# Optimization experiments

Hardware: AMD Instinct MI355X
Metric: run time of the kernel (lower is better)

## Reference

```python
import jax, jax.numpy as jnp
import numpy as np

B, T, D = 2, 2048, 1024
H, HD = 16, 64
DL, DC = 512, 256
THETA = 10000.0
LN_EPS = 1e-5


def setup_inputs() -> dict:
    key = jax.random.key(0)
    ks = jax.random.split(key, 8)
    s = 0.02
    return {
        "x": jax.random.normal(ks[0], (B, T, D), jnp.float32),
        "W_q": jax.random.normal(ks[1], (H * HD, D), jnp.float32) * s,
        "b_q": jnp.zeros((H * HD,), jnp.float32),
        "W_kvl": jax.random.normal(ks[2], (DL, D), jnp.float32) * s,
        "b_kvl": jnp.zeros((DL,), jnp.float32),
        "ts_scale": jnp.ones((DL,), jnp.float32),
        "ts_shift": jnp.zeros((DL,), jnp.float32),
        "W_comp": jax.random.normal(ks[3], (DC, DL), jnp.float32) * s,
        "W_exp": jax.random.normal(ks[4], (DL, DC), jnp.float32) * s,
        "ln_g": jnp.ones((DC,), jnp.float32),
        "ln_b": jnp.zeros((DC,), jnp.float32),
        "W_fkv": jax.random.normal(ks[5], (2 * H * HD, DL), jnp.float32) * s,
        "b_fkv": jnp.zeros((2 * H * HD,), jnp.float32),
        "W_out": jax.random.normal(ks[6], (D, H * HD), jnp.float32) * s,
        "b_out": jnp.zeros((D,), jnp.float32),
    }


def _rope_tables(t_len):
    inv_freq = 1.0 / (THETA ** (jnp.arange(0, HD, 2, dtype=jnp.float32) / HD))
    pos = jnp.arange(t_len, dtype=jnp.float32)
    freqs = pos[:, None] * inv_freq[None, :]          # [T, HD/2]
    cos = jnp.concatenate([jnp.cos(freqs)] * 2, -1)   # [T, HD]
    sin = jnp.concatenate([jnp.sin(freqs)] * 2, -1)
    return cos[None, None], sin[None, None]           # [1,1,T,HD]


def _rotate_half(z):
    return jnp.concatenate([-z[..., HD // 2:], z[..., :HD // 2]], -1)


def reference(x, W_q, b_q, W_kvl, b_kvl, ts_scale, ts_shift, W_comp, W_exp,
              ln_g, ln_b, W_fkv, b_fkv, W_out, b_out):
    # Q path: [B,T,D] -> [B,H,T,HD]
    q = (jnp.einsum('btd,ed->bte', x, W_q) + b_q).reshape(B, T, H, HD).transpose(0, 2, 1, 3)

    # KV latent + learned KVSplice bottleneck
    kvl = jnp.einsum('btd,ld->btl', x, W_kvl) + b_kvl                 # [B,T,DL]
    xt = kvl * jax.nn.softplus(ts_scale) + ts_shift
    c = jnp.einsum('btl,cl->btc', xt, W_comp)                         # [B,T,DC]
    mu = jnp.mean(c, -1, keepdims=True)
    var = jnp.mean(jnp.square(c - mu), -1, keepdims=True)
    c = (c - mu) * jax.lax.rsqrt(var + LN_EPS) * ln_g + ln_b
    dec = jnp.einsum('btc,lc->btl', c, W_exp)                         # [B,T,DL]

    # Decompress latent to K,V
    kv = jnp.einsum('btl,el->bte', dec, W_fkv) + b_fkv                # [B,T,2*H*HD]
    kv = kv.reshape(B, T, 2, H, HD).transpose(2, 0, 3, 1, 4)          # [2,B,H,T,HD]
    k, v = kv[0], kv[1]

    # RoPE
    cos, sin = _rope_tables(T)
    q = q * cos + _rotate_half(q) * sin
    k = k * cos + _rotate_half(k) * sin

    # Causal SDPA
    scale = 1.0 / np.sqrt(HD)
    scores = jnp.einsum('bhqd,bhkd->bhqk', q, k) * scale
    mask = jnp.tril(jnp.ones((T, T), bool))
    scores = jnp.where(mask, scores, jnp.float32(-1e30))
    attn = jax.nn.softmax(scores, axis=-1)
    o = jnp.einsum('bhqk,bhkd->bhqd', attn, v)
    o = o.transpose(0, 2, 1, 3).reshape(B, T, H * HD)
    return jnp.einsum('bte,de->btd', o, W_out) + b_out
```

## Files before the change

### kernel.cpp

```cpp
#include <hip/hip_runtime.h>
#include <math.h>

#define B_SZ   2
#define T_SEQ  2048
#define NH     16
#define HDIM   64
#define D_MOD  1024
#define DL     512
#define DC     256
#define MROWS  4096

typedef __attribute__((ext_vector_type(8))) short bf16x8;
typedef __attribute__((ext_vector_type(4))) float f32x4;

#define SCALE_Q 0.18033688011112042f

static __device__ __forceinline__ unsigned short f2bf(float f) {
    union { float f; unsigned u; } v; v.f = f;
    unsigned r = v.u + 0x7fffu + ((v.u >> 16) & 1u);
    return (unsigned short)(r >> 16);
}

static __device__ __forceinline__ void gl_lds16(const unsigned short* g,
                                                unsigned short* l) {
    __builtin_amdgcn_global_load_lds(
        (const __attribute__((address_space(1))) unsigned int*)g,
        (__attribute__((address_space(3))) unsigned int*)l, 16, 0, 0);
}

__global__ __launch_bounds__(256) void cvt_bf16(
    const float* __restrict__ x,  const float* __restrict__ wq,
    const float* __restrict__ wkvl, const float* __restrict__ wcomp,
    const float* __restrict__ wexp, const float* __restrict__ wfkv,
    const float* __restrict__ wout,
    unsigned short* __restrict__ xb,  unsigned short* __restrict__ wqh,
    unsigned short* __restrict__ wkvlh, unsigned short* __restrict__ wcomph,
    unsigned short* __restrict__ wexph, unsigned short* __restrict__ wfkvh,
    unsigned short* __restrict__ wouth, float2* __restrict__ rope_tab)
{
    const int g = blockIdx.x * 256 + threadIdx.x;
    const int stride = gridDim.x * 256;
#define CVT_SEG(src, dst, n4)                                              \
    for (int i = g; i < (n4); i += stride) {                               \
        float4 v = ((const float4*)(src))[i];                              \
        unsigned short h[4] = {f2bf(v.x), f2bf(v.y), f2bf(v.z), f2bf(v.w)};\
        *(uint2*)((dst) + (size_t)i * 4) = *(uint2*)h;                     \
    }
    CVT_SEG(x, xb, 1048576)
    CVT_SEG(wq, wqh, 262144)
    CVT_SEG(wkvl, wkvlh, 131072)
    CVT_SEG(wcomp, wcomph, 32768)
    CVT_SEG(wexp, wexph, 32768)
    CVT_SEG(wfkv, wfkvh, 262144)
    CVT_SEG(wout, wouth, 262144)
#undef CVT_SEG
    for (int i = g; i < T_SEQ * 32; i += stride) {
        const int t = i >> 5, fi = i & 31;
        const float inv = __expf((float)fi * (-9.210340371976184f / 32.0f));
        float sn, cs; sincosf((float)t * inv, &sn, &cs);
        rope_tab[i] = make_float2(cs, sn);
    }
}

#define GEMM64R_PROLOG(Aptr, Wptr, Kdim)                                       \
    __shared__ unsigned short As[64 * 64];                                     \
    __shared__ unsigned short Ws[64 * 64];                                     \
    const int tid = threadIdx.x;                                               \
    const int w = tid >> 6, lane = tid & 63;                                   \
    const int l16 = lane & 15, quad = lane >> 4;                               \
    const int sw8 = ((lane & 7) ^ ((lane >> 3) & 7)) << 3;                     \
    const int srow = lane >> 3;                                                \
    const unsigned short* Ag0 = (Aptr) + (size_t)(m0 + w * 16 + srow) * (Kdim) + sw8;      \
    const unsigned short* Ag1 = (Aptr) + (size_t)(m0 + w * 16 + 8 + srow) * (Kdim) + sw8;  \
    const unsigned short* Wg0 = (Wptr) + (size_t)(n0 + w * 16 + srow) * (Kdim) + sw8;      \
    const unsigned short* Wg1 = (Wptr) + (size_t)(n0 + w * 16 + 8 + srow) * (Kdim) + sw8;  \
    unsigned short* Al0 = &As[(w * 16) * 64];                                  \
    unsigned short* Al1 = &As[(w * 16 + 8) * 64];                              \
    unsigned short* Wl0 = &Ws[(w * 16) * 64];                                  \
    unsigned short* Wl1 = &Ws[(w * 16 + 8) * 64];                              \
    const int xh = (l16 & 7);                                                  \
    f32x4 acc[4];                                                              \
    _Pragma("unroll") for (int j = 0; j < 4; ++j)                              \
        acc[j] = (f32x4){0.f, 0.f, 0.f, 0.f};                                  \
    for (int k0 = 0; k0 < (Kdim); k0 += 64) {                                  \
        __syncthreads();                                                       \
        gl_lds16(Ag0 + k0, Al0);                                               \
        gl_lds16(Ag1 + k0, Al1);                                               \
        gl_lds16(Wg0 + k0, Wl0);                                               \
        gl_lds16(Wg1 + k0, Wl1);                                               \
        __syncthreads();                                                       \
        bf16x8 af[2], bfr[4][2];                                               \
        _Pragma("unroll") for (int kk = 0; kk < 2; ++kk)                       \
            af[kk] = *(const bf16x8*)&As[(w * 16 + l16) * 64 +                 \
                                         (((kk * 4 + quad) ^ xh) << 3)];       \
        _Pragma("unroll") for (int j = 0; j < 4; ++j)                          \
            _Pragma("unroll") for (int kk = 0; kk < 2; ++kk)                   \
                bfr[j][kk] = *(const bf16x8*)&Ws[(j * 16 + l16) * 64 +         \
                                             (((kk * 4 + quad) ^ xh) << 3)];   \
        _Pragma("unroll") for (int kk = 0; kk < 2; ++kk)                       \
            _Pragma("unroll") for (int j = 0; j < 4; ++j)                      \
                acc[j] = __builtin_amdgcn_mfma_f32_16x16x32_bf16(              \
                    af[kk], bfr[j][kk], acc[j], 0, 0, 0);                      \
    }

__global__ __launch_bounds__(256) void gemm_qxt(
    const unsigned short* __restrict__ A, const unsigned short* __restrict__ Wq,
    const unsigned short* __restrict__ Wkvl,
    const float* __restrict__ b_q, const float* __restrict__ b_kvl,
    const float* __restrict__ ts_scale, const float* __restrict__ ts_shift,
    const float2* __restrict__ tab,
    unsigned short* __restrict__ qh, unsigned short* __restrict__ xt)
{
    const int m0 = blockIdx.x * 64;
    const bool is_q = (blockIdx.y < 16);
    const int n0 = is_q ? blockIdx.y * 64 : (blockIdx.y - 16) * 64;
    const unsigned short* W = is_q ? Wq : Wkvl;

    GEMM64R_PROLOG(A, W, D_MOD)

    if (is_q) {
#pragma unroll
        for (int j = 0; j < 4; ++j) {
            const int col = n0 + j * 16 + l16;
            const int h = col >> 6, hd = col & 63;
            const float bv = b_q[col];
            const float bvp = b_q[col ^ 32];
            const float sgn = (hd < 32) ? -1.f : 1.f;
#pragma unroll
            for (int reg = 0; reg < 4; ++reg) {
                const int row = m0 + w * 16 + quad * 4 + reg;
                const int b = row >> 11, t = row & (T_SEQ - 1);
                const float2 cssn = tab[t * 32 + (hd & 31)];
                const float v  = acc[j][reg] + bv;
                const float vp = acc[j ^ 2][reg] + bvp;
                const float r = (v * cssn.x + sgn * vp * cssn.y) * SCALE_Q;
                qh[(((size_t)b * NH + h) * T_SEQ + t) * HDIM + hd] = f2bf(r);
            }
        }
    } else {
#pragma unroll
        for (int j = 0; j < 4; ++j) {
            const int col = n0 + j * 16 + l16;
            const float bv = b_kvl[col];
            const float sp_s = log1pf(expf(ts_scale[col]));
            const float sp_t = ts_shift[col];
#pragma unroll
            for (int reg = 0; reg < 4; ++reg) {
                const int row = m0 + w * 16 + quad * 4 + reg;
                const float val = (acc[j][reg] + bv) * sp_s + sp_t;
                xt[(size_t)row * DL + col] = f2bf(val);
            }
        }
    }
}

__global__ __launch_bounds__(256) void gemm_kv(
    const unsigned short* __restrict__ A, const unsigned short* __restrict__ W,
    const float* __restrict__ bias, const float2* __restrict__ tab,
    unsigned short* __restrict__ kh, unsigned short* __restrict__ vth)
{
    const int m0 = blockIdx.x * 64, n0 = blockIdx.y * 64;

    GEMM64R_PROLOG(A, W, DL)

    if (n0 < 1024) {
#pragma unroll
        for (int j = 0; j < 4; ++j) {
            const int col = n0 + j * 16 + l16;
            const int h = (col >> 6) & 15, hd = col & 63;
            const float bv = bias[col];
            const float bvp = bias[col ^ 32];
            const float sgn = (hd < 32) ? -1.f : 1.f;
#pragma unroll
            for (int reg = 0; reg < 4; ++reg) {
                const int row = m0 + w * 16 + quad * 4 + reg;
                const int b = row >> 11, t = row & (T_SEQ - 1);
                const float2 cssn = tab[t * 32 + (hd & 31)];
                const float v  = acc[j][reg] + bv;
                const float vp = acc[j ^ 2][reg] + bvp;
                const float r = v * cssn.x + sgn * vp * cssn.y;
                kh[(((size_t)b * NH + h) * T_SEQ + t) * HDIM + hd] = f2bf(r);
            }
        }
    } else {
#pragma unroll
        for (int j = 0; j < 4; ++j) {
            const int col = n0 + j * 16 + l16;
            const int cv = col - 1024;
            const int h = cv >> 6, hd = cv & 63;
            const float bv = bias[col];
            unsigned short hv[4];
            const int r0 = m0 + w * 16 + quad * 4;
            const int b = r0 >> 11, t0 = r0 & (T_SEQ - 1);
#pragma unroll
            for (int reg = 0; reg < 4; ++reg)
                hv[reg] = f2bf(acc[j][reg] + bv);
            *(uint2*)&vth[(((size_t)b * NH + h) * HDIM + hd) * T_SEQ + t0] =
                *(uint2*)hv;
        }
    }
}

__global__ __launch_bounds__(256) void gemm_out(
    const unsigned short* __restrict__ A, const unsigned short* __restrict__ W,
    const float* __restrict__ bias, float* __restrict__ C)
{
    const int m0 = blockIdx.x * 64, n0 = blockIdx.y * 64;

    GEMM64R_PROLOG(A, W, D_MOD)

#pragma unroll
    for (int j = 0; j < 4; ++j) {
        const int col = n0 + j * 16 + l16;
        const float bv = bias[col];
#pragma unroll
        for (int reg = 0; reg < 4; ++reg) {
            const int row = m0 + w * 16 + quad * 4 + reg;
            C[(size_t)row * D_MOD + col] = acc[j][reg] + bv;
        }
    }
}

__global__ __launch_bounds__(256) void gemm_b(
    const unsigned short* __restrict__ A, const unsigned short* __restrict__ W,
    unsigned short* __restrict__ dec)
{
    const int m0 = blockIdx.x * 64, n0 = blockIdx.y * 64;

    GEMM64R_PROLOG(A, W, DC)

#pragma unroll
    for (int j = 0; j < 4; ++j) {
        const int col = n0 + j * 16 + l16;
#pragma unroll
        for (int reg = 0; reg < 4; ++reg) {
            const int row = m0 + w * 16 + quad * 4 + reg;
            dec[(size_t)row * DL + col] = f2bf(acc[j][reg]);
        }
    }
}

__global__ __launch_bounds__(256) void gemm_c_ln(
    const unsigned short* __restrict__ A, const unsigned short* __restrict__ W,
    const float* __restrict__ g, const float* __restrict__ bta,
    unsigned short* __restrict__ outb)
{
    __shared__ unsigned short As[16 * 32];
    __shared__ unsigned short Ws[256 * 32];
    __shared__ float redS[4][16];
    __shared__ float redQ[4][16];

    const int tid = threadIdx.x;
    const int w = tid >> 6, lane = tid & 63;
    const int l16 = lane & 15, quad = lane >> 4;
    const int m0 = blockIdx.x * 16;

    const int srow = lane >> 2, scol = (lane & 3) << 3;
    const unsigned short* Ag = A + (size_t)(m0 + srow) * DL + scol;
    const unsigned short* Wg = W + (size_t)(w * 64 + srow) * DL + scol;

    f32x4 acc[4];
#pragma unroll
    for (int j = 0; j < 4; ++j) acc[j] = (f32x4){0.f, 0.f, 0.f, 0.f};

    for (int k0 = 0; k0 < DL; k0 += 32) {
        __syncthreads();
        if (w == 0) gl_lds16(Ag + k0, &As[0]);
#pragma unroll
        for (int c = 0; c < 4; ++c)
            gl_lds16(Wg + (size_t)(c * 16) * DL + k0, &Ws[(w * 64 + c * 16) * 32]);
        __syncthreads();

        const bf16x8 af = *(const bf16x8*)&As[l16 * 32 + quad * 8];
        bf16x8 bfr[4];
#pragma unroll
        for (int j = 0; j < 4; ++j)
            bfr[j] = *(const bf16x8*)&Ws[(w * 64 + j * 16 + l16) * 32 + quad * 8];
#pragma unroll
        for (int j = 0; j < 4; ++j)
            acc[j] = __builtin_amdgcn_mfma_f32_16x16x32_bf16(af, bfr[j], acc[j], 0, 0, 0);
    }

    float s[4], q2[4];
#pragma unroll
    for (int reg = 0; reg < 4; ++reg) {
        float sv = (acc[0][reg] + acc[1][reg]) + (acc[2][reg] + acc[3][reg]);
        float qv = (acc[0][reg] * acc[0][reg] + acc[1][reg] * acc[1][reg]) +
                   (acc[2][reg] * acc[2][reg] + acc[3][reg] * acc[3][reg]);
#pragma unroll
        for (int off = 1; off < 16; off <<= 1) {
            sv += __shfl_xor(sv, off);
            qv += __shfl_xor(qv, off);
        }
        s[reg] = sv; q2[reg] = qv;
    }
    if (l16 == 0) {
#pragma unroll
        for (int reg = 0; reg < 4; ++reg) {
            redS[w][quad * 4 + reg] = s[reg];
            redQ[w][quad * 4 + reg] = q2[reg];
        }
    }
    __syncthreads();

#pragma unroll
    for (int reg = 0; reg < 4; ++reg) {
        const int r = quad * 4 + reg;
        const float sum = (redS[0][r] + redS[1][r]) + (redS[2][r] + redS[3][r]);
        const float sq  = (redQ[0][r] + redQ[1][r]) + (redQ[2][r] + redQ[3][r]);
        const float mu  = sum * (1.0f / DC);
        const float var = sq * (1.0f / DC) - mu * mu;
        const float rstd = rsqrtf(var + 1e-5f);
#pragma unroll
        for (int j = 0; j < 4; ++j) {
            const int col = w * 64 + j * 16 + l16;
            const float val = (acc[j][reg] - mu) * rstd * g[col] + bta[col];
            outb[(size_t)(m0 + r) * DC + col] = f2bf(val);
        }
    }
}

__global__ __launch_bounds__(256, 3) void flash_mfma(
    const unsigned short* __restrict__ q, const unsigned short* __restrict__ k,
    const unsigned short* __restrict__ vt, unsigned short* __restrict__ o)
{
    __shared__ unsigned short Ks[64 * 72];
    __shared__ unsigned short Vs[64 * 72];
    __shared__ unsigned short Ps[64 * 72];

    const int bh = blockIdx.x & 31;
    const int j  = 31 - (blockIdx.x >> 5);
    const int q0 = j * 64;
    const int tid = threadIdx.x;
    const int w = tid >> 6, lane = tid & 63;
    const int l16 = lane & 15, quad = lane >> 4;
    const int rbase = q0 + w * 16;

    bf16x8 qf[2];
#pragma unroll
    for (int kk = 0; kk < 2; ++kk)
        qf[kk] = *(const bf16x8*)(q + ((size_t)bh * T_SEQ + rbase + l16) * HDIM + kk * 32 + quad * 8);

    f32x4 of[4];
    float lrow[4];
#pragma unroll
    for (int dt = 0; dt < 4; ++dt) of[dt] = (f32x4){0.f, 0.f, 0.f, 0.f};
#pragma unroll
    for (int r = 0; r < 4; ++r) lrow[r] = 0.f;

    const int ldr = tid >> 2;
    const int ldc = (tid & 3) * 16;
    const unsigned short* kgb = k + ((size_t)bh * T_SEQ + ldr) * HDIM + ldc;
    const unsigned short* vgb = vt + ((size_t)bh * HDIM + ldr) * T_SEQ + ldc;

    const int kend = (j + 1) * 64;
    for (int k0 = 0; k0 < kend; k0 += 64) {
        __syncthreads();
        {
            const unsigned short* kg = kgb + (size_t)k0 * HDIM;
            *(bf16x8*)&Ks[ldr * 72 + ldc]     = *(const bf16x8*)kg;
            *(bf16x8*)&Ks[ldr * 72 + ldc + 8] = *(const bf16x8*)(kg + 8);
            const unsigned short* vg = vgb + k0;
            *(bf16x8*)&Vs[ldr * 72 + ldc]     = *(const bf16x8*)vg;
            *(bf16x8*)&Vs[ldr * 72 + ldc + 8] = *(const bf16x8*)(vg + 8);
        }
        __syncthreads();

        bf16x8 kf[4][2];
#pragma unroll
        for (int nt = 0; nt < 4; ++nt)
#pragma unroll
            for (int kk = 0; kk < 2; ++kk)
                kf[nt][kk] = *(const bf16x8*)&Ks[(nt * 16 + l16) * 72 + kk * 32 + quad * 8];

        f32x4 sf[4];
#pragma unroll
        for (int nt = 0; nt < 4; ++nt) {
            sf[nt] = (f32x4){0.f, 0.f, 0.f, 0.f};
#pragma unroll
            for (int kk = 0; kk < 2; ++kk)
                sf[nt] = __builtin_amdgcn_mfma_f32_16x16x32_bf16(qf[kk], kf[nt][kk], sf[nt], 0, 0, 0);
        }

        const bool need_mask = (k0 + 63) > rbase;
#pragma unroll
        for (int reg = 0; reg < 4; ++reg) {
            float a0 = sf[0][reg], a1 = sf[1][reg], a2 = sf[2][reg], a3 = sf[3][reg];
            if (need_mask) {
                const int tq = rbase + quad * 4 + reg;
                if (k0 +      l16 > tq) a0 = -1e30f;
                if (k0 + 16 + l16 > tq) a1 = -1e30f;
                if (k0 + 32 + l16 > tq) a2 = -1e30f;
                if (k0 + 48 + l16 > tq) a3 = -1e30f;
            }
            union { float f; unsigned u; } u0, u1, u2, u3;
            u0.f = exp2f(a0); u1.f = exp2f(a1);
            u2.f = exp2f(a2); u3.f = exp2f(a3);
            const int prow = (w * 16 + quad * 4 + reg) * 72 + l16;
            Ps[prow]      = (unsigned short)(u0.u >> 16);
            Ps[prow + 16] = (unsigned short)(u1.u >> 16);
            Ps[prow + 32] = (unsigned short)(u2.u >> 16);
            Ps[prow + 48] = (unsigned short)(u3.u >> 16);
            u0.u &= 0xffff0000u; u1.u &= 0xffff0000u;
            u2.u &= 0xffff0000u; u3.u &= 0xffff0000u;
            lrow[reg] += (u0.f + u1.f) + (u2.f + u3.f);
        }

        bf16x8 vf[4][2];
#pragma unroll
        for (int dt = 0; dt < 4; ++dt)
#pragma unroll
            for (int kk = 0; kk < 2; ++kk)
                vf[dt][kk] = *(const bf16x8*)&Vs[(dt * 16 + l16) * 72 + kk * 32 + quad * 8];

        bf16x8 pf[2];
#pragma unroll
        for (int kk = 0; kk < 2; ++kk)
            pf[kk] = *(const bf16x8*)&Ps[(w * 16 + l16) * 72 + kk * 32 + quad * 8];
#pragma unroll
        for (int dt = 0; dt < 4; ++dt)
#pragma unroll
            for (int kk = 0; kk < 2; ++kk)
                of[dt] = __builtin_amdgcn_mfma_f32_16x16x32_bf16(pf[kk], vf[dt][kk], of[dt], 0, 0, 0);
    }

    const int b = bh >> 4, h = bh & 15;
#pragma unroll
    for (int reg = 0; reg < 4; ++reg) {
        float l = lrow[reg];
        l += __shfl_xor(l, 1);
        l += __shfl_xor(l, 2);
        l += __shfl_xor(l, 4);
        l += __shfl_xor(l, 8);
        const float inv = 1.0f / l;
        const int t = rbase + quad * 4 + reg;
#pragma unroll
        for (int dt = 0; dt < 4; ++dt)
            o[((size_t)b * T_SEQ + t) * (NH * HDIM) + h * HDIM + dt * 16 + l16] =
                f2bf(of[dt][reg] * inv);
    }
}

extern "C" void kernel_launch(void* const* d_in, const int* in_sizes, int n_in,
                              void* d_out, int out_size, void* d_ws, size_t ws_size,
                              hipStream_t stream)
{
    (void)in_sizes; (void)n_in; (void)out_size; (void)ws_size;

    const float* x        = (const float*)d_in[0];
    const float* W_q      = (const float*)d_in[1];
    const float* b_q      = (const float*)d_in[2];
    const float* W_kvl    = (const float*)d_in[3];
    const float* b_kvl    = (const float*)d_in[4];
    const float* ts_scale = (const float*)d_in[5];
    const float* ts_shift = (const float*)d_in[6];
    const float* W_comp   = (const float*)d_in[7];
    const float* W_exp    = (const float*)d_in[8];
    const float* ln_g     = (const float*)d_in[9];
    const float* ln_b     = (const float*)d_in[10];
    const float* W_fkv    = (const float*)d_in[11];
    const float* b_fkv    = (const float*)d_in[12];
    const float* W_out    = (const float*)d_in[13];
    const float* b_out    = (const float*)d_in[14];
    float* out = (float*)d_out;

    char* p = (char*)d_ws;
    unsigned short* xb     = (unsigned short*)p;             p += 8  * 1024 * 1024;
    unsigned short* wqh    = (unsigned short*)p;             p += 2  * 1024 * 1024;
    unsigned short* wkvlh  = (unsigned short*)p;             p += 1  * 1024 * 1024;
    unsigned short* wcomph = (unsigned short*)p;             p += 256 * 1024;
    unsigned short* wexph  = (unsigned short*)p;             p += 256 * 1024;
    unsigned short* wfkvh  = (unsigned short*)p;             p += 2  * 1024 * 1024;
    unsigned short* wouth  = (unsigned short*)p;             p += 2  * 1024 * 1024;
    unsigned short* qh     = (unsigned short*)p;             p += 8  * 1024 * 1024;
    unsigned short* kh     = (unsigned short*)p;             p += 8  * 1024 * 1024;
    unsigned short* vth    = (unsigned short*)p;             p += 8  * 1024 * 1024;
    unsigned short* xt     = (unsigned short*)p;             p += 4  * 1024 * 1024;
    unsigned short* cbh    = (unsigned short*)p;             p += 2  * 1024 * 1024;
    unsigned short* dec    = (unsigned short*)p;             p += 4  * 1024 * 1024;
    unsigned short* ob     = (unsigned short*)p;             p += 8  * 1024 * 1024;
    float2*         tab    = (float2*)p;                     p += 512 * 1024;

    const dim3 blk(256);

    cvt_bf16<<<1024, blk, 0, stream>>>(x, W_q, W_kvl, W_comp, W_exp, W_fkv, W_out,
                                       xb, wqh, wkvlh, wcomph, wexph, wfkvh, wouth,
                                       tab);

    gemm_qxt<<<dim3(64, 24), blk, 0, stream>>>(
        xb, wqh, wkvlh, b_q, b_kvl, ts_scale, ts_shift, tab, qh, xt);

    gemm_c_ln<<<256, blk, 0, stream>>>(
        xt, wcomph, ln_g, ln_b, cbh);

    gemm_b<<<dim3(64, 8), blk, 0, stream>>>(
        cbh, wexph, dec);

    gemm_kv<<<dim3(64, 32), blk, 0, stream>>>(
        dec, wfkvh, b_fkv, tab, kh, vth);

    flash_mfma<<<1024, blk, 0, stream>>>(qh, kh, vth, ob);

    gemm_out<<<dim3(64, 16), blk, 0, stream>>>(
        ob, wouth, b_out, out);
}
```

Measured before the change: 220.9 us.

## Move Q projection into KV GEMM launch, widen LN GEMM k-step, rebalance flash order

The Q projection leaves the first GEMM and is merged into the K/V decompression GEMM launch. The serial chain xt→c→dec now carries fewer blocks, and the K/V launch gets more blocks to fill the GPU. The compress+LayerNorm GEMM now loads 64-wide k-tiles with an XOR-swizzled LDS layout, which halves its loop iterations and reduces bank conflicts. The flash attention block order is changed to interleave heavy and light causal query tiles so the load is better balanced across waves.

Result: no change. 222.8 us (+0.8%).

```diff
diff --git a/kernel.cpp b/kernel.cpp
--- a/kernel.cpp
+++ b/kernel.cpp
@@ -62,9 +62,11 @@
     }
 }
 
+#define GEMM64R_SHARED                                                         \
+    __shared__ unsigned short As[64 * 64];                                     \
+    __shared__ unsigned short Ws[64 * 64];
+
 #define GEMM64R_PROLOG(Aptr, Wptr, Kdim)                                       \
-    __shared__ unsigned short As[64 * 64];                                     \
-    __shared__ unsigned short Ws[64 * 64];                                     \
     const int tid = threadIdx.x;                                               \
     const int w = tid >> 6, lane = tid & 63;                                   \
     const int l16 = lane & 15, quad = lane >> 4;                               \
@@ -103,101 +105,105 @@
                     af[kk], bfr[j][kk], acc[j], 0, 0, 0);                      \
     }
 
-__global__ __launch_bounds__(256) void gemm_qxt(
-    const unsigned short* __restrict__ A, const unsigned short* __restrict__ Wq,
-    const unsigned short* __restrict__ Wkvl,
-    const float* __restrict__ b_q, const float* __restrict__ b_kvl,
+#define Q_EPILOGUE                                                             \
+    _Pragma("unroll") for (int j = 0; j < 4; ++j) {                            \
+        const int col = n0 + j * 16 + l16;                                     \
+        const int h = col >> 6, hd = col & 63;                                 \
+        const float bv = b_q[col];                                             \
+        const float bvp = b_q[col ^ 32];                                       \
+        const float sgn = (hd < 32) ? -1.f : 1.f;                              \
+        _Pragma("unroll") for (int reg = 0; reg < 4; ++reg) {                  \
+            const int row = m0 + w * 16 + quad * 4 + reg;                      \
+            const int b = row >> 11, t = row & (T_SEQ - 1);                    \
+            const float2 cssn = tab[t * 32 + (hd & 31)];                       \
+            const float v  = acc[j][reg] + bv;                                 \
+            const float vp = acc[j ^ 2][reg] + bvp;                            \
+            const float r = (v * cssn.x + sgn * vp * cssn.y) * SCALE_Q;        \
+            qh[(((size_t)b * NH + h) * T_SEQ + t) * HDIM + hd] = f2bf(r);      \
+        }                                                                      \
+    }
+
+__global__ __launch_bounds__(256) void gemm_xt(
+    const unsigned short* __restrict__ A, const unsigned short* __restrict__ W,
+    const float* __restrict__ b_kvl,
     const float* __restrict__ ts_scale, const float* __restrict__ ts_shift,
-    const float2* __restrict__ tab,
-    unsigned short* __restrict__ qh, unsigned short* __restrict__ xt)
-{
+    unsigned short* __restrict__ xt)
+{
+    GEMM64R_SHARED
+    const int m0 = blockIdx.x * 64, n0 = blockIdx.y * 64;
+
+    GEMM64R_PROLOG(A, W, D_MOD)
+
+#pragma unroll
+    for (int j = 0; j < 4; ++j) {
+        const int col = n0 + j * 16 + l16;
+        const float bv = b_kvl[col];
+        const float sp_s = log1pf(expf(ts_scale[col]));
+        const float sp_t = ts_shift[col];
+#pragma unroll
+        for (int reg = 0; reg < 4; ++reg) {
+            const int row = m0 + w * 16 + quad * 4 + reg;
+            const float val = (acc[j][reg] + bv) * sp_s + sp_t;
+            xt[(size_t)row * DL + col] = f2bf(val);
+        }
+    }
+}
+
+__global__ __launch_bounds__(256) void gemm_kvq(
+    const unsigned short* __restrict__ dec, const unsigned short* __restrict__ Wfkv,
+    const float* __restrict__ b_fkv,
+    const unsigned short* __restrict__ xb, const unsigned short* __restrict__ Wq,
+    const float* __restrict__ b_q, const float2* __restrict__ tab,
+    unsigned short* __restrict__ kh, unsigned short* __restrict__ vth,
+    unsigned short* __restrict__ qh)
+{
+    GEMM64R_SHARED
     const int m0 = blockIdx.x * 64;
-    const bool is_q = (blockIdx.y < 16);
-    const int n0 = is_q ? blockIdx.y * 64 : (blockIdx.y - 16) * 64;
-    const unsigned short* W = is_q ? Wq : Wkvl;
-
-    GEMM64R_PROLOG(A, W, D_MOD)
-
-    if (is_q) {
-#pragma unroll
-        for (int j = 0; j < 4; ++j) {
-            const int col = n0 + j * 16 + l16;
-            const int h = col >> 6, hd = col & 63;
-            const float bv = b_q[col];
-            const float bvp = b_q[col ^ 32];
-            const float sgn = (hd < 32) ? -1.f : 1.f;
-#pragma unroll
-            for (int reg = 0; reg < 4; ++reg) {
-                const int row = m0 + w * 16 + quad * 4 + reg;
-                const int b = row >> 11, t = row & (T_SEQ - 1);
-                const float2 cssn = tab[t * 32 + (hd & 31)];
-                const float v  = acc[j][reg] + bv;
-                const float vp = acc[j ^ 2][reg] + bvp;
-                const float r = (v * cssn.x + sgn * vp * cssn.y) * SCALE_Q;
-                qh[(((size_t)b * NH + h) * T_SEQ + t) * HDIM + hd] = f2bf(r);
+    const int y = blockIdx.y;
+
+    if (y < 32) {
+        const int n0 = y * 64;
+        GEMM64R_PROLOG(dec, Wfkv, DL)
+        if (n0 < 1024) {
+#pragma unroll
+            for (int j = 0; j < 4; ++j) {
+                const int col = n0 + j * 16 + l16;
+                const int h = (col >> 6) & 15, hd = col & 63;
+                const float bv = b_fkv[col];
+                const float bvp = b_fkv[col ^ 32];
+                const float sgn = (hd < 32) ? -1.f : 1.f;
+#pragma unroll
+                for (int reg = 0; reg < 4; ++reg) {
+                    const int row = m0 + w * 16 + quad * 4 + reg;
+                    const int b = row >> 11, t = row & (T_SEQ - 1);
+                    const float2 cssn = tab[t * 32 + (hd & 31)];
+                    const float v  = acc[j][reg] + bv;
+                    const float vp = acc[j ^ 2][reg] + bvp;
+                    const float r = v * cssn.x + sgn * vp * cssn.y;
+                    kh[(((size_t)b * NH + h) * T_SEQ + t) * HDIM + hd] = f2bf(r);
+                }
             }
+        } else {
+#pragma unroll
+            for (int j = 0; j < 4; ++j) {
+                const int col = n0 + j * 16 + l16;
+                const int cv = col - 1024;
+                const int h = cv >> 6, hd = cv & 63;
+                const float bv = b_fkv[col];
+                unsigned short hv[4];
+                const int r0 = m0 + w * 16 + quad * 4;
+                const int b = r0 >> 11, t0 = r0 & (T_SEQ - 1);
+#pragma unroll
+                for (int reg = 0; reg < 4; ++reg)
+                    hv[reg] = f2bf(acc[j][reg] + bv);
+                *(uint2*)&vth[(((size_t)b * NH + h) * HDIM + hd) * T_SEQ + t0] =
+                    *(uint2*)hv;
+            }
         }
     } else {
-#pragma unroll
-        for (int j = 0; j < 4; ++j) {
-            const int col = n0 + j * 16 + l16;
-            const float bv = b_kvl[col];
-            const float sp_s = log1pf(expf(ts_scale[col]));
-            const float sp_t = ts_shift[col];
-#pragma unroll
-            for (int reg = 0; reg < 4; ++reg) {
-                const int row = m0 + w * 16 + quad * 4 + reg;
-                const float val = (acc[j][reg] + bv) * sp_s + sp_t;
-                xt[(size_t)row * DL + col] = f2bf(val);
-            }
-        }
-    }
-}
-
-__global__ __launch_bounds__(256) void gemm_kv(
-    const unsigned short* __restrict__ A, const unsigned short* __restrict__ W,
-    const float* __restrict__ bias, const float2* __restrict__ tab,
-    unsigned short* __restrict__ kh, unsigned short* __restrict__ vth)
-{
-    const int m0 = blockIdx.x * 64, n0 = blockIdx.y * 64;
-
-    GEMM64R_PROLOG(A, W, DL)
-
-    if (n0 < 1024) {
-#pragma unroll
-        for (int j = 0; j < 4; ++j) {
-            const int col = n0 + j * 16 + l16;
-            const int h = (col >> 6) & 15, hd = col & 63;
-            const float bv = bias[col];
-            const float bvp = bias[col ^ 32];
-            const float sgn = (hd < 32) ? -1.f : 1.f;
-#pragma unroll
-            for (int reg = 0; reg < 4; ++reg) {
-                const int row = m0 + w * 16 + quad * 4 + reg;
-                const int b = row >> 11, t = row & (T_SEQ - 1);
-                const float2 cssn = tab[t * 32 + (hd & 31)];
-                const float v  = acc[j][reg] + bv;
-                const float vp = acc[j ^ 2][reg] + bvp;
-                const float r = v * cssn.x + sgn * vp * cssn.y;
-                kh[(((size_t)b * NH + h) * T_SEQ + t) * HDIM + hd] = f2bf(r);
-            }
-        }
-    } else {
-#pragma unroll
-        for (int j = 0; j < 4; ++j) {
-            const int col = n0 + j * 16 + l16;
-            const int cv = col - 1024;
-            const int h = cv >> 6, hd = cv & 63;
-            const float bv = bias[col];
-            unsigned short hv[4];
-            const int r0 = m0 + w * 16 + quad * 4;
-            const int b = r0 >> 11, t0 = r0 & (T_SEQ - 1);
-#pragma unroll
-            for (int reg = 0; reg < 4; ++reg)
-                hv[reg] = f2bf(acc[j][reg] + bv);
-            *(uint2*)&vth[(((size_t)b * NH + h) * HDIM + hd) * T_SEQ + t0] =
-                *(uint2*)hv;
-        }
+        const int n0 = (y - 32) * 64;
+        GEMM64R_PROLOG(xb, Wq, D_MOD)
+        Q_EPILOGUE
     }
 }
 
@@ -205,6 +211,7 @@
     const unsigned short* __restrict__ A, const unsigned short* __restrict__ W,
     const float* __restrict__ bias, float* __restrict__ C)
 {
+    GEMM64R_SHARED
     const int m0 = blockIdx.x * 64, n0 = blockIdx.y * 64;
 
     GEMM64R_PROLOG(A, W, D_MOD)
@@ -225,6 +232,7 @@
     const unsigned short* __restrict__ A, const unsigned short* __restrict__ W,
     unsigned short* __restrict__ dec)
 {
+    GEMM64R_SHARED
     const int m0 = blockIdx.x * 64, n0 = blockIdx.y * 64;
 
     GEMM64R_PROLOG(A, W, DC)
@@ -245,8 +253,8 @@
     const float* __restrict__ g, const float* __restrict__ bta,
     unsigned short* __restrict__ outb)
 {
-    __shared__ unsigned short As[16 * 32];
-    __shared__ unsigned short Ws[256 * 32];
+    __shared__ unsigned short As[16 * 64];
+    __shared__ unsigned short Ws[256 * 64];
     __shared__ float redS[4][16];
     __shared__ float redQ[4][16];
 
@@ -255,30 +263,45 @@
     const int l16 = lane & 15, quad = lane >> 4;
     const int m0 = blockIdx.x * 16;
 
-    const int srow = lane >> 2, scol = (lane & 3) << 3;
-    const unsigned short* Ag = A + (size_t)(m0 + srow) * DL + scol;
-    const unsigned short* Wg = W + (size_t)(w * 64 + srow) * DL + scol;
+    const int sw8 = ((lane & 7) ^ ((lane >> 3) & 7)) << 3;
+    const int srow = lane >> 3;
+    const int xh = (l16 & 7);
+
+    const unsigned short* Ag0 = A + (size_t)(m0 + srow) * DL + sw8;
+    const unsigned short* Ag1 = A + (size_t)(m0 + 8 + srow) * DL + sw8;
 
     f32x4 acc[4];
 #pragma unroll
     for (int j = 0; j < 4; ++j) acc[j] = (f32x4){0.f, 0.f, 0.f, 0.f};
 
-    for (int k0 = 0; k0 < DL; k0 += 32) {
+    for (int k0 = 0; k0 < DL; k0 += 64) {
         __syncthreads();
-        if (w == 0) gl_lds16(Ag + k0, &As[0]);
-#pragma unroll
-        for (int c = 0; c < 4; ++c)
-            gl_lds16(Wg + (size_t)(c * 16) * DL + k0, &Ws[(w * 64 + c * 16) * 32]);
+        if (w == 0) {
+            gl_lds16(Ag0 + k0, &As[0]);
+            gl_lds16(Ag1 + k0, &As[8 * 64]);
+        }
+#pragma unroll
+        for (int c = 0; c < 8; ++c)
+            gl_lds16(W + (size_t)(w * 64 + c * 8 + srow) * DL + k0 + sw8,
+                     &Ws[(w * 64 + c * 8) * 64]);
         __syncthreads();
 
-        const bf16x8 af = *(const bf16x8*)&As[l16 * 32 + quad * 8];
-        bf16x8 bfr[4];
+        bf16x8 af[2], bfr[4][2];
+#pragma unroll
+        for (int kk = 0; kk < 2; ++kk)
+            af[kk] = *(const bf16x8*)&As[l16 * 64 + (((kk * 4 + quad) ^ xh) << 3)];
 #pragma unroll
         for (int j = 0; j < 4; ++j)
-            bfr[j] = *(const bf16x8*)&Ws[(w * 64 + j * 16 + l16) * 32 + quad * 8];
-#pragma unroll
-        for (int j = 0; j < 4; ++j)
-            acc[j] = __builtin_amdgcn_mfma_f32_16x16x32_bf16(af, bfr[j], acc[j], 0, 0, 0);
+#pragma unroll
+            for (int kk = 0; kk < 2; ++kk)
+                bfr[j][kk] = *(const bf16x8*)&Ws[(w * 64 + j * 16 + l16) * 64 +
+                                                 (((kk * 4 + quad) ^ xh) << 3)];
+#pragma unroll
+        for (int kk = 0; kk < 2; ++kk)
+#pragma unroll
+            for (int j = 0; j < 4; ++j)
+                acc[j] = __builtin_amdgcn_mfma_f32_16x16x32_bf16(
+                    af[kk], bfr[j][kk], acc[j], 0, 0, 0);
     }
 
     float s[4], q2[4];
@@ -328,8 +351,12 @@
     __shared__ unsigned short Vs[64 * 72];
     __shared__ unsigned short Ps[64 * 72];
 
-    const int bh = blockIdx.x & 31;
-    const int j  = 31 - (blockIdx.x >> 5);
+    const int g  = blockIdx.x >> 8;
+    const int c  = blockIdx.x & 255;
+    const int s  = c >> 5;
+    const int bh = c & 31;
+    const int j  = (g == 0) ? (31 - s) : (g == 1) ? (16 + s)
+                 : (g == 2) ? (15 - s) : s;
     const int q0 = j * 64;
     const int tid = threadIdx.x;
     const int w = tid >> 6, lane = tid & 63;
@@ -487,8 +514,8 @@
                                        xb, wqh, wkvlh, wcomph, wexph, wfkvh, wouth,
                                        tab);
 
-    gemm_qxt<<<dim3(64, 24), blk, 0, stream>>>(
-        xb, wqh, wkvlh, b_q, b_kvl, ts_scale, ts_shift, tab, qh, xt);
+    gemm_xt<<<dim3(64, 8), blk, 0, stream>>>(
+        xb, wkvlh, b_kvl, ts_scale, ts_shift, xt);
 
     gemm_c_ln<<<256, blk, 0, stream>>>(
         xt, wcomph, ln_g, ln_b, cbh);
@@ -496,8 +523,8 @@
     gemm_b<<<dim3(64, 8), blk, 0, stream>>>(
         cbh, wexph, dec);
 
-    gemm_kv<<<dim3(64, 32), blk, 0, stream>>>(
-        dec, wfkvh, b_fkv, tab, kh, vth);
+    gemm_kvq<<<dim3(64, 48), blk, 0, stream>>>(
+        dec, wfkvh, b_fkv, xb, wqh, b_q, tab, kh, vth, qh);
 
     flash_mfma<<<1024, blk, 0, stream>>>(qh, kh, vth, ob);
 
```
